# Kernel optimization log

Hardware: AMD Instinct MI355X
Metric: run time of the kernel (lower is better)

Reference implementation:

```python
import jax, jax.numpy as jnp
import numpy as np

EPS = 1e-5

def conv1d_same(x, w, b):
    # x: [B,C,T], w: [O,I,K], b: [O]
    y = jax.lax.conv_general_dilated(x, w, window_strides=(1,), padding='SAME',
                                     dimension_numbers=('NCH', 'OIH', 'NCH'))
    return y + b[None, :, None]

def bn_eval(x, gamma, beta):
    # running_mean=0, running_var=1 (fresh BatchNorm1d in eval mode)
    inv = 1.0 / jnp.sqrt(1.0 + EPS)
    return x * (gamma * inv)[None, :, None] + beta[None, :, None]

def gelu(x):
    return jax.nn.gelu(x, approximate=False)

def conv_block(x, c1w, c1b, c2w, c2b, g1, be1, g2, be2, skw=None, skb=None):
    res = x if skw is None else jnp.einsum('bct,oc->bot', x, skw[:, :, 0]) + skb[None, :, None]
    h = gelu(bn_eval(conv1d_same(x, c1w, c1b), g1, be1))
    h = bn_eval(conv1d_same(h, c2w, c2b), g2, be2)
    return gelu(h + res)

def setup_inputs() -> dict:
    key = jax.random.key(0)
    ks = jax.random.split(key, 32)
    B, C, T = 1024, 271, 281
    H, H2, E, NCLS, NSUBJ = 128, 256, 16, 1854, 4
    g = lambda i, shape, s=0.02: jax.random.normal(ks[i], shape, dtype=jnp.float32) * s
    inp = {}
    inp['X'] = jax.random.normal(ks[0], (B, C, T), dtype=jnp.float32)
    inp['subject_idxs'] = jax.random.randint(ks[1], (B,), 0, NSUBJ, dtype=jnp.int32)
    inp['attention'] = jax.random.normal(ks[2], (C, C), dtype=jnp.float32)
    inp['sa_w'] = g(3, (H, C), 0.05)
    inp['sa_b'] = jnp.zeros((H,), jnp.float32)
    inp['subj_w'] = g(4, (NSUBJ, H, H), 0.05)
    inp['subj_b'] = jnp.zeros((NSUBJ, H), jnp.float32)
    # block1: 128->128 (identity skip)
    inp['b1_c1w'] = g(5, (H, H, 3)); inp['b1_c1b'] = jnp.zeros((H,), jnp.float32)
    inp['b1_c2w'] = g(6, (H, H, 3)); inp['b1_c2b'] = jnp.zeros((H,), jnp.float32)
    inp['b1_g1'] = jnp.ones((H,), jnp.float32); inp['b1_be1'] = jnp.zeros((H,), jnp.float32)
    inp['b1_g2'] = jnp.ones((H,), jnp.float32); inp['b1_be2'] = jnp.zeros((H,), jnp.float32)
    # block2: 128->256 (1x1 conv skip)
    inp['b2_c1w'] = g(7, (H2, H, 3)); inp['b2_c1b'] = jnp.zeros((H2,), jnp.float32)
    inp['b2_c2w'] = g(8, (H2, H2, 3)); inp['b2_c2b'] = jnp.zeros((H2,), jnp.float32)
    inp['b2_g1'] = jnp.ones((H2,), jnp.float32); inp['b2_be1'] = jnp.zeros((H2,), jnp.float32)
    inp['b2_g2'] = jnp.ones((H2,), jnp.float32); inp['b2_be2'] = jnp.zeros((H2,), jnp.float32)
    inp['b2_skw'] = g(9, (H2, H, 1)); inp['b2_skb'] = jnp.zeros((H2,), jnp.float32)
    # block3: 256->256 (identity skip)
    inp['b3_c1w'] = g(10, (H2, H2, 3)); inp['b3_c1b'] = jnp.zeros((H2,), jnp.float32)
    inp['b3_c2w'] = g(11, (H2, H2, 3)); inp['b3_c2b'] = jnp.zeros((H2,), jnp.float32)
    inp['b3_g1'] = jnp.ones((H2,), jnp.float32); inp['b3_be1'] = jnp.zeros((H2,), jnp.float32)
    inp['b3_g2'] = jnp.ones((H2,), jnp.float32); inp['b3_be2'] = jnp.zeros((H2,), jnp.float32)
    # subject embedding + head
    inp['emb'] = g(12, (NSUBJ, E), 1.0)
    inp['head_w1'] = g(13, (H, H2 + E), 0.05); inp['head_b1'] = jnp.zeros((H,), jnp.float32)
    inp['head_w2'] = g(14, (NCLS, H), 0.05); inp['head_b2'] = jnp.zeros((NCLS,), jnp.float32)
    return inp

def reference(X, subject_idxs, attention, sa_w, sa_b, subj_w, subj_b,
              b1_c1w, b1_c1b, b1_c2w, b1_c2b, b1_g1, b1_be1, b1_g2, b1_be2,
              b2_c1w, b2_c1b, b2_c2w, b2_c2b, b2_g1, b2_be1, b2_g2, b2_be2, b2_skw, b2_skb,
              b3_c1w, b3_c1b, b3_c2w, b3_c2b, b3_g1, b3_be1, b3_g2, b3_be2,
              emb, head_w1, head_b1, head_w2, head_b2):
    # SpatialAttention
    attn = jax.nn.softmax(attention, axis=1)            # [C,C]
    x = jnp.einsum('bct,ic->bit', X, attn)              # [B,C,T]
    x = jnp.einsum('bit,oi->bot', x, sa_w) + sa_b[None, :, None]  # [B,H,T]
    # Per-subject 1x1 conv: batched gather of weights instead of python loop
    Ws = subj_w[subject_idxs]                           # [B,H,H]
    bs = subj_b[subject_idxs]                           # [B,H]
    x = jnp.einsum('bct,boc->bot', x, Ws) + bs[:, :, None]
    # ConvBlock stack
    x = conv_block(x, b1_c1w, b1_c1b, b1_c2w, b1_c2b, b1_g1, b1_be1, b1_g2, b1_be2)
    x = conv_block(x, b2_c1w, b2_c1b, b2_c2w, b2_c2b, b2_g1, b2_be1, b2_g2, b2_be2, b2_skw, b2_skb)
    x = conv_block(x, b3_c1w, b3_c1b, b3_c2w, b3_c2b, b3_g1, b3_be1, b3_g2, b3_be2)
    # Head: global avg pool over time, concat subject embedding, MLP
    x = jnp.mean(x, axis=2)                             # [B,2H]
    x = jnp.concatenate([x, emb[subject_idxs]], axis=1) # [B,2H+E]
    h = jax.nn.relu(x @ head_w1.T + head_b1)
    return h @ head_w2.T + head_b2                      # [B,num_classes]
```

## Files before the change

kernel.cpp:

```cpp
#include <hip/hip_runtime.h>
#include <hip/hip_bf16.h>
#include <math.h>

constexpr int Bz = 1024;
constexpr int C0 = 271;
constexpr int CP0 = 288;
constexpr int Tt = 281;
constexpr int TR = 292;
constexpr int H1 = 128;
constexpr int H2 = 256;
constexpr int NCLS = 1854;
constexpr int ED = 16;
constexpr float BN_INV = 0.9999950000374996f;

typedef __attribute__((ext_vector_type(8))) short s16x8;
typedef __attribute__((ext_vector_type(16))) float f32x16;

__device__ __forceinline__ float gelu_f(float v) {
    return 0.5f * v * (1.0f + erff(v * 0.7071067811865475f));
}
__device__ __forceinline__ float bf2f(short s) {
    return __builtin_bit_cast(float, ((unsigned int)(unsigned short)s) << 16);
}
__device__ __forceinline__ short f2bf(float f) {
    return __builtin_bit_cast(short, __float2bfloat16(f));
}

typedef unsigned int u32;
typedef const __attribute__((address_space(1))) u32 gu32;
typedef __attribute__((address_space(3))) u32 lu32;

__device__ __forceinline__ void gl16(const void* g, void* l) {
    __builtin_amdgcn_global_load_lds((gu32*)(uintptr_t)g, (lu32*)(uintptr_t)l, 16, 0, 0);
}
template<int N> __device__ __forceinline__ void waitv() {
    asm volatile("s_waitcnt vmcnt(%0)" :: "i"(N) : "memory");
}
__device__ __forceinline__ void hard_barrier() {
    __builtin_amdgcn_s_barrier();
    __builtin_amdgcn_sched_barrier(0);
}


__global__ void zrows_k(short* base, int C) {
    const int b = blockIdx.x;
    const int n = 11 * (C / 8);
    for (int i = threadIdx.x; i < n; i += 256) {
        int ri = i / (C / 8), c8 = i - ri * (C / 8);
        int row = (ri == 0) ? 0 : 281 + ri;
        *(int4*)(base + ((size_t)b * TR + row) * C + c8 * 8) = make_int4(0, 0, 0, 0);
    }
}

__global__ void softmax_rows_k(const float* __restrict__ a, float* __restrict__ o, int n) {
    __shared__ float red[256];
    const int row = blockIdx.x, tid = threadIdx.x;
    const float* r = a + (size_t)row * n;
    float m = -1e30f;
    for (int i = tid; i < n; i += 256) m = fmaxf(m, r[i]);
    red[tid] = m; __syncthreads();
    for (int s = 128; s > 0; s >>= 1) { if (tid < s) red[tid] = fmaxf(red[tid], red[tid + s]); __syncthreads(); }
    m = red[0]; __syncthreads();
    float acc = 0.f;
    for (int i = tid; i < n; i += 256) acc += expf(r[i] - m);
    red[tid] = acc; __syncthreads();
    for (int s = 128; s > 0; s >>= 1) { if (tid < s) red[tid] += red[tid + s]; __syncthreads(); }
    const float inv = 1.0f / red[0];
    for (int i = tid; i < n; i += 256) o[(size_t)row * n + i] = expf(r[i] - m) * inv;
}

__global__ void gemm_M_k(const float* __restrict__ sa_w, const float* __restrict__ attnS,
                         float* __restrict__ M) {
    int idx = blockIdx.x * 256 + threadIdx.x;
    if (idx >= H1 * C0) return;
    int o = idx / C0, c = idx - o * C0;
    float s = 0.f;
    for (int i = 0; i < C0; ++i) s = fmaf(sa_w[(size_t)o * C0 + i], attnS[(size_t)i * C0 + c], s);
    M[idx] = s;
}

__global__ void wfrag_k(const float* __restrict__ w, short* __restrict__ out,
                        int CIN, int O, int K, int NC) {
    int idx = blockIdx.x * 256 + threadIdx.x;
    int OB32 = O / 32;
    int total = NC * K * OB32 * 2 * 512;
    if (idx >= total) return;
    int j = idx & 7, lane = (idx >> 3) & 63, kk = (idx >> 9) & 1, r = idx >> 10;
    int ob = r % OB32, r2 = r / OB32;
    int k = r2 % K, cc = r2 / K;
    int o = ob * 32 + (lane & 31);
    int c = cc * 32 + kk * 16 + (lane >> 5) * 8 + j;
    float v = (c < CIN) ? w[((size_t)o * CIN + c) * K + k] : 0.f;
    out[idx] = f2bf(v);
}

__global__ void msubA_k(const float* __restrict__ subj_w, const float* __restrict__ M,
                        short* __restrict__ out) {
    int idx = blockIdx.x * 256 + threadIdx.x;
    const int per_s = 9 * 1 * 4 * 2 * 512;
    if (idx >= 4 * per_s) return;
    int s = idx / per_s, rem = idx % per_s;
    int j = rem & 7, lane = (rem >> 3) & 63, kk = (rem >> 9) & 1, r = rem >> 10;
    int ob = r % 4, cc = r / 4;
    int o = ob * 32 + (lane & 31);
    int c = cc * 32 + kk * 16 + (lane >> 5) * 8 + j;
    float a = 0.f;
    if (c < C0) {
        const float* wr = subj_w + ((size_t)s * 128 + o) * 128;
        for (int h = 0; h < 128; ++h) a = fmaf(wr[h], M[(size_t)h * C0 + c], a);
    }
    out[idx] = f2bf(a);
}

__global__ void biasS_k(const float* __restrict__ subj_w, const float* __restrict__ sa_b,
                        const float* __restrict__ subj_b, float* __restrict__ biasS) {
    int idx = blockIdx.x * 256 + threadIdx.x;
    if (idx >= 4 * H1) return;
    int s = idx >> 7, o = idx & 127;
    const float* wr = subj_w + ((size_t)s * H1 + o) * H1;
    float a = subj_b[idx];
    for (int h = 0; h < H1; ++h) a = fmaf(wr[h], sa_b[h], a);
    biasS[idx] = a;
}

__global__ void xpose_k(const float* __restrict__ X, short* __restrict__ xT) {
    __shared__ float tile[32][33];
    int b = blockIdx.z;
    int t0 = blockIdx.x * 32, c0 = blockIdx.y * 32;
    int tx = threadIdx.x, ty = threadIdx.y;
    #pragma unroll
    for (int i = 0; i < 4; ++i) {
        int c = c0 + ty + i * 8, t = t0 + tx;
        float v = 0.f;
        if (c < C0 && t < Tt) v = X[((size_t)b * C0 + c) * Tt + t];
        tile[ty + i * 8][tx] = v;
    }
    __syncthreads();
    #pragma unroll
    for (int i = 0; i < 4; ++i) {
        int t = t0 + ty + i * 8, c = c0 + tx;
        if (t < Tt) xT[((size_t)b * TR + t + 1) * CP0 + c] = f2bf(tile[tx][ty + i * 8]);
    }
}


template<int NCCp, int ROWUp, int NW, int NCH>
__device__ __forceinline__ void convFS_stage(
    const short* slabg, int XC, int cubase, char* lds, int wv, int lane)
{
    constexpr int ROWB = ROWUp * 16;
    for (int i = wv; i < NCH; i += NW) {
        int pos = i * 1024 + lane * 16;
        int rl = pos / ROWB;
        int up = (pos - rl * ROWB) >> 4;
        if (rl > 291) rl = 291;
        int ul = up ^ (rl & 7);
        int srcu = (ul < NCCp * 4) ? ul : 0;
        gl16(slabg + (size_t)rl * XC + (cubase + srcu) * 8, lds + i * 1024);
    }
}

template<int K, int NCCp, int ROWUp, int OB32>
__device__ __forceinline__ void convFS_compute(
    f32x16 (&acc)[2][3], const short* __restrict__ wb, const char* Xb,
    int ccbase, int tg, int lane, int l31, int hi, int wvo)
{
    constexpr int ROWB = ROWUp * 16;
    constexpr int ROFF = 1 - (K - 1) / 2;
    #pragma unroll
    for (int cc = 0; cc < NCCp; ++cc) {
        s16x8 a[2][K][2];
        #pragma unroll
        for (int os = 0; os < 2; ++os)
            #pragma unroll
            for (int k = 0; k < K; ++k)
                #pragma unroll
                for (int kk = 0; kk < 2; ++kk) {
                    int ci = (((ccbase + cc) * K + k) * OB32 + wvo * 2 + os) * 2 + kk;
                    a[os][k][kk] = *(const s16x8*)(wb + (size_t)ci * 512 + lane * 8);
                }
        #pragma unroll
        for (int k = 0; k < K; ++k)
            #pragma unroll
            for (int kk = 0; kk < 2; ++kk)
                #pragma unroll
                for (int ts = 0; ts < 3; ++ts) {
                    int rl = tg + ts * 32 + l31 + k + ROFF;
                    s16x8 bv = *(const s16x8*)(Xb + (size_t)rl * ROWB +
                        (((cc * 4 + (kk << 1) + hi) ^ (rl & 7)) << 4));
                    acc[0][ts] = __builtin_amdgcn_mfma_f32_32x32x16_bf16(a[0][k][kk], bv, acc[0][ts], 0, 0, 0);
                    acc[1][ts] = __builtin_amdgcn_mfma_f32_32x32x16_bf16(a[1][k][kk], bv, acc[1][ts], 0, 0, 0);
                }
    }
}

template<int K, int NCC_A, int ROWU_A, int NCC_B, int ROWU_B,
         int O_BLK, int NOW, int NB, bool GELU, bool HASRES>
__global__ __launch_bounds__(NOW * NB * 192)
void convFS(const short* __restrict__ xin, int XC,
            const short* __restrict__ wfrag,
            const float* __restrict__ bias,
            const float* __restrict__ gamma, const float* __restrict__ beta,
            const short* __restrict__ res, short* __restrict__ out,
            const int* __restrict__ sidx, int wsub, int bsub)
{
    constexpr int NW    = NOW * NB * 3;
    constexpr int NT    = NW * 64;
    constexpr int OB32  = O_BLK / 32;
    constexpr int SLABB = ((292 * ROWU_A * 16) + 1023) & ~1023;
    constexpr int NCH_A = SLABB / 1024;
    constexpr int NCH_B = (292 * ROWU_B * 16 + 1023) / 1024;
    constexpr int O2    = O_BLK * 2;

    __shared__ __align__(16) char smem[NB * SLABB];

    const int b0   = blockIdx.x * NB;
    const int tid  = threadIdx.x;
    const int lane = tid & 63, wv = tid >> 6;
    const int l31  = lane & 31, hi = lane >> 5;
    const int bqw  = wv / (NOW * 3);
    const int w2   = wv % (NOW * 3);
    const int wvt  = w2 / NOW;
    const int wvo  = w2 % NOW;
    const int tg   = wvt * 96;

    int subj = sidx ? sidx[b0] : 0;
    const short* wb = wfrag + (size_t)subj * wsub;
    const float* bb = bias + (size_t)subj * bsub;

    f32x16 acc[2][3];
    #pragma unroll
    for (int i = 0; i < 2; ++i)
        #pragma unroll
        for (int j = 0; j < 3; ++j)
            #pragma unroll
            for (int e = 0; e < 16; ++e) acc[i][j][e] = 0.f;

    #pragma unroll
    for (int b = 0; b < NB; ++b)
        convFS_stage<NCC_A, ROWU_A, NW, NCH_A>(
            xin + (size_t)(b0 + b) * TR * XC, XC, 0, smem + b * SLABB, wv, lane);
    waitv<0>();
    hard_barrier();

    const char* Xb = smem + bqw * SLABB;
    convFS_compute<K, NCC_A, ROWU_A, OB32>(acc, wb, Xb, 0, tg, lane, l31, hi, wvo);

    if constexpr (NCC_B > 0) {
        hard_barrier();
        #pragma unroll
        for (int b = 0; b < NB; ++b)
            convFS_stage<NCC_B, ROWU_B, NW, NCH_B>(
                xin + (size_t)(b0 + b) * TR * XC, XC, NCC_A * 4, smem + b * SLABB, wv, lane);
        waitv<0>();
        hard_barrier();
        convFS_compute<K, NCC_B, ROWU_B, OB32>(acc, wb, Xb, NCC_A, tg, lane, l31, hi, wvo);
    }

    constexpr int RCH = O_BLK / 8;
    for (int g = 0; g < 3; ++g) {
        __syncthreads();
        if (wvt == g) {
            #pragma unroll
            for (int os = 0; os < 2; ++os) {
                #pragma unroll
                for (int rq = 0; rq < 4; ++rq) {
                    #pragma unroll
                    for (int rp = 0; rp < 2; ++rp) {
                        const int oc = wvo * 64 + os * 32 + 8 * rq + rp * 2 + 4 * hi;
                        const float bv0 = bb[oc], bv1 = bb[oc + 1];
                        const float g0 = gamma ? gamma[oc] * BN_INV : 1.f;
                        const float g1 = gamma ? gamma[oc + 1] * BN_INV : 1.f;
                        const float e0 = beta ? beta[oc] : 0.f;
                        const float e1 = beta ? beta[oc + 1] : 0.f;
                        const int r0 = rq * 4 + rp * 2;
                        #pragma unroll
                        for (int ts = 0; ts < 3; ++ts) {
                            float v0 = (acc[os][ts][r0] + bv0) * g0 + e0;
                            float v1 = (acc[os][ts][r0 + 1] + bv1) * g1 + e1;
                            int tl = ts * 32 + l31;
                            int byte = (bqw * 96 + tl) * O2 + ((oc * 2) ^ ((tl & 15) << 4));
                            __hip_bfloat162 pk;
                            pk.x = __float2bfloat16(v0);
                            pk.y = __float2bfloat16(v1);
                            *(__hip_bfloat162*)(smem + byte) = pk;
                        }
                    }
                }
            }
        }
        __syncthreads();
        for (int qq = tid; qq < NB * 96 * RCH; qq += NT) {
            int bql = qq / (96 * RCH), rem = qq - bql * (96 * RCH);
            int r = rem / RCH, cp = rem - r * RCH;
            int t = g * 96 + r;
            if (t >= Tt) continue;
            s16x8 hv = *(const s16x8*)(smem + (bql * 96 + r) * O2 + ((cp * 16) ^ ((r & 15) << 4)));
            size_t orow = ((size_t)(b0 + bql) * TR + t + 1) * O_BLK + cp * 8;
            s16x8 rv;
            if (HASRES) rv = *(const s16x8*)(res + orow);
            s16x8 ov;
            #pragma unroll
            for (int j = 0; j < 8; ++j) {
                float v = bf2f(hv[j]);
                if (HASRES) v += bf2f(rv[j]);
                if (GELU) v = gelu_f(v);
                ov[j] = f2bf(v);
            }
            *(s16x8*)(out + orow) = ov;
        }
    }
}


__global__ void poolCL_k(const short* __restrict__ x, float* __restrict__ pooled) {
    const int b = blockIdx.x;
    const int o = threadIdx.x;
    const short* p = x + ((size_t)b * TR + 1) * H2 + o;
    float s = 0.f;
    for (int t = 0; t < Tt; ++t) s += bf2f(p[(size_t)t * H2]);
    pooled[(size_t)b * H2 + o] = s * (1.0f / Tt);
}

__global__ void head1_k(const float* __restrict__ pooled, const float* __restrict__ emb,
                        const int* __restrict__ sidx, const float* __restrict__ w1,
                        const float* __restrict__ b1, float* __restrict__ hout) {
    int idx = blockIdx.x * 256 + threadIdx.x;
    if (idx >= Bz * H1) return;
    int b = idx >> 7, j = idx & 127;
    const float* wr = w1 + (size_t)j * (H2 + ED);
    const float* pr = pooled + (size_t)b * H2;
    float a = b1[j];
    for (int i = 0; i < H2; ++i) a = fmaf(pr[i], wr[i], a);
    const float* er = emb + (size_t)sidx[b] * ED;
    #pragma unroll
    for (int e = 0; e < ED; ++e) a = fmaf(er[e], wr[H2 + e], a);
    hout[idx] = fmaxf(a, 0.f);
}

__global__ __launch_bounds__(256)
void head2_k(const float* __restrict__ h, const float* __restrict__ w2,
             const float* __restrict__ b2, float* __restrict__ out) {
    const int n0 = blockIdx.x * 64;
    const int b0 = blockIdx.y * 16;
    __shared__ float hs[16][128];
    __shared__ float w2s[64][129];
    const int tid = threadIdx.x;
    for (int idx = tid; idx < 16 * 128; idx += 256) {
        int bl = idx >> 7, j = idx & 127;
        hs[bl][j] = h[(size_t)(b0 + bl) * H1 + j];
    }
    for (int idx = tid; idx < 64 * 128; idx += 256) {
        int nl = idx >> 7, j = idx & 127;
        int n = n0 + nl;
        w2s[nl][j] = (n < NCLS) ? w2[(size_t)n * H1 + j] : 0.f;
    }
    __syncthreads();
    const int nl = tid & 63, bg = tid >> 6;
    float acc[4] = {0.f, 0.f, 0.f, 0.f};
    for (int j = 0; j < 128; ++j) {
        const float wv = w2s[nl][j];
        #pragma unroll
        for (int bb = 0; bb < 4; ++bb) acc[bb] = fmaf(wv, hs[bg * 4 + bb][j], acc[bb]);
    }
    const int n = n0 + nl;
    if (n < NCLS) {
        const float bv = b2[n];
        #pragma unroll
        for (int bb = 0; bb < 4; ++bb)
            out[(size_t)(b0 + bg * 4 + bb) * NCLS + n] = acc[bb] + bv;
    }
}


extern "C" void kernel_launch(void* const* d_in, const int* in_sizes, int n_in,
                              void* d_out, int out_size, void* d_ws, size_t ws_size,
                              hipStream_t stream) {
    const float* X      = (const float*)d_in[0];
    const int*   sidx   = (const int*)  d_in[1];
    const float* attn   = (const float*)d_in[2];
    const float* sa_w   = (const float*)d_in[3];
    const float* sa_b   = (const float*)d_in[4];
    const float* subj_w = (const float*)d_in[5];
    const float* subj_b = (const float*)d_in[6];
    const float* b1c1w = (const float*)d_in[7];  const float* b1c1b = (const float*)d_in[8];
    const float* b1c2w = (const float*)d_in[9];  const float* b1c2b = (const float*)d_in[10];
    const float* b1g1  = (const float*)d_in[11]; const float* b1be1 = (const float*)d_in[12];
    const float* b1g2  = (const float*)d_in[13]; const float* b1be2 = (const float*)d_in[14];
    const float* b2c1w = (const float*)d_in[15]; const float* b2c1b = (const float*)d_in[16];
    const float* b2c2w = (const float*)d_in[17]; const float* b2c2b = (const float*)d_in[18];
    const float* b2g1  = (const float*)d_in[19]; const float* b2be1 = (const float*)d_in[20];
    const float* b2g2  = (const float*)d_in[21]; const float* b2be2 = (const float*)d_in[22];
    const float* b2skw = (const float*)d_in[23]; const float* b2skb = (const float*)d_in[24];
    const float* b3c1w = (const float*)d_in[25]; const float* b3c1b = (const float*)d_in[26];
    const float* b3c2w = (const float*)d_in[27]; const float* b3c2b = (const float*)d_in[28];
    const float* b3g1  = (const float*)d_in[29]; const float* b3be1 = (const float*)d_in[30];
    const float* b3g2  = (const float*)d_in[31]; const float* b3be2 = (const float*)d_in[32];
    const float* emb   = (const float*)d_in[33];
    const float* hw1   = (const float*)d_in[34]; const float* hb1 = (const float*)d_in[35];
    const float* hw2   = (const float*)d_in[36]; const float* hb2 = (const float*)d_in[37];
    float* out = (float*)d_out;
    (void)in_sizes; (void)n_in; (void)out_size; (void)ws_size;

    char* wsp = (char*)d_ws;
    size_t off = 0;
    auto allocF = [&](size_t n) {
        float* p = (float*)(wsp + off);
        off += ((n * sizeof(float)) + 255) & ~(size_t)255;
        return p;
    };
    auto allocS = [&](size_t n) {
        short* p = (short*)(wsp + off);
        off += ((n * sizeof(short)) + 255) & ~(size_t)255;
        return p;
    };
    float* attnS   = allocF((size_t)C0 * C0);
    float* Mmat    = allocF((size_t)H1 * C0);
    float* biasS   = allocF((size_t)4 * H1);
    float* pooled  = allocF((size_t)Bz * H2);
    float* hbuf    = allocF((size_t)Bz * H1);
    short* wStageA = allocS((size_t)4 * 9 * 4 * 2 * 512);
    short* wp_b1c1 = allocS((size_t)4 * 3 * 4 * 2 * 512);
    short* wp_b1c2 = allocS((size_t)4 * 3 * 4 * 2 * 512);
    short* wp_skip = allocS((size_t)4 * 1 * 8 * 2 * 512);
    short* wp_b2c1 = allocS((size_t)4 * 3 * 8 * 2 * 512);
    short* wp_b2c2 = allocS((size_t)8 * 3 * 8 * 2 * 512);
    short* wp_b3c1 = allocS((size_t)8 * 3 * 8 * 2 * 512);
    short* wp_b3c2 = allocS((size_t)8 * 3 * 8 * 2 * 512);
    short* xT   = allocS((size_t)Bz * TR * CP0);
    short* bufP = allocS((size_t)Bz * TR * H1);
    short* bufQ = allocS((size_t)Bz * TR * H1);
    short* bufR = allocS((size_t)Bz * TR * H2);
    short* bufS = allocS((size_t)Bz * TR * H2);

    zrows_k<<<Bz, 256, 0, stream>>>(xT, CP0);
    zrows_k<<<Bz, 256, 0, stream>>>(bufP, H1);
    zrows_k<<<Bz, 256, 0, stream>>>(bufQ, H1);
    zrows_k<<<Bz, 256, 0, stream>>>(bufR, H2);
    zrows_k<<<Bz, 256, 0, stream>>>(bufS, H2);

    softmax_rows_k<<<C0, 256, 0, stream>>>(attn, attnS, C0);
    gemm_M_k<<<(H1 * C0 + 255) / 256, 256, 0, stream>>>(sa_w, attnS, Mmat);
    msubA_k<<<(4 * 36864 + 255) / 256, 256, 0, stream>>>(subj_w, Mmat, wStageA);
    biasS_k<<<2, 256, 0, stream>>>(subj_w, sa_b, subj_b, biasS);
    wfrag_k<<<(4*3*4*2*512 + 255) / 256, 256, 0, stream>>>(b1c1w, wp_b1c1, 128, 128, 3, 4);
    wfrag_k<<<(4*3*4*2*512 + 255) / 256, 256, 0, stream>>>(b1c2w, wp_b1c2, 128, 128, 3, 4);
    wfrag_k<<<(4*1*8*2*512 + 255) / 256, 256, 0, stream>>>(b2skw, wp_skip, 128, 256, 1, 4);
    wfrag_k<<<(4*3*8*2*512 + 255) / 256, 256, 0, stream>>>(b2c1w, wp_b2c1, 128, 256, 3, 4);
    wfrag_k<<<(8*3*8*2*512 + 255) / 256, 256, 0, stream>>>(b2c2w, wp_b2c2, 256, 256, 3, 8);
    wfrag_k<<<(8*3*8*2*512 + 255) / 256, 256, 0, stream>>>(b3c1w, wp_b3c1, 256, 256, 3, 8);
    wfrag_k<<<(8*3*8*2*512 + 255) / 256, 256, 0, stream>>>(b3c2w, wp_b3c2, 256, 256, 3, 8);
    xpose_k<<<dim3(9, 9, Bz), dim3(32, 8), 0, stream>>>(X, xT);

    convFS<1, 5, 24, 4, 16, 128, 2, 1, false, false><<<Bz, 384, 0, stream>>>(
        xT, CP0, wStageA, biasS, nullptr, nullptr, nullptr, bufP, sidx, 36864, 128);
    convFS<3, 4, 16, 0, 0, 128, 2, 2, true, false><<<Bz / 2, 768, 0, stream>>>(
        bufP, H1, wp_b1c1, b1c1b, b1g1, b1be1, nullptr, bufQ, nullptr, 0, 0);
    convFS<3, 4, 16, 0, 0, 128, 2, 2, true, true><<<Bz / 2, 768, 0, stream>>>(
        bufQ, H1, wp_b1c2, b1c2b, b1g2, b1be2, bufP, bufP, nullptr, 0, 0);
    convFS<1, 4, 16, 0, 0, 256, 4, 1, false, false><<<Bz, 768, 0, stream>>>(
        bufP, H1, wp_skip, b2skb, nullptr, nullptr, nullptr, bufS, nullptr, 0, 0);
    convFS<3, 4, 16, 0, 0, 256, 4, 1, true, false><<<Bz, 768, 0, stream>>>(
        bufP, H1, wp_b2c1, b2c1b, b2g1, b2be1, nullptr, bufR, nullptr, 0, 0);
    convFS<3, 8, 32, 0, 0, 256, 4, 1, true, true><<<Bz, 768, 0, stream>>>(
        bufR, H2, wp_b2c2, b2c2b, b2g2, b2be2, bufS, bufS, nullptr, 0, 0);
    convFS<3, 8, 32, 0, 0, 256, 4, 1, true, false><<<Bz, 768, 0, stream>>>(
        bufS, H2, wp_b3c1, b3c1b, b3g1, b3be1, nullptr, bufR, nullptr, 0, 0);
    convFS<3, 8, 32, 0, 0, 256, 4, 1, true, true><<<Bz, 768, 0, stream>>>(
        bufR, H2, wp_b3c2, b3c2b, b3g2, b3be2, bufS, bufS, nullptr, 0, 0);

    poolCL_k<<<Bz, 256, 0, stream>>>(bufS, pooled);
    head1_k<<<(Bz * H1 + 255) / 256, 256, 0, stream>>>(pooled, emb, sidx, hw1, hb1, hbuf);
    head2_k<<<dim3((NCLS + 63) / 64, Bz / 16), 256, 0, stream>>>(hbuf, hw2, hb2, out);
}
```

Baseline: 1.370 ms.

## Tile conv kernels over time chunks and fuse final conv with average pooling

Replaces the whole-sequence conv kernel with a kernel that splits each sample's time axis into three 96-step tiles on a second grid dimension, so each block stages only a 104-row halo slab in LDS. This uses smaller blocks with a launch bound of two per CU to raise occupancy, and issues the MFMA sequences under raised wave priority. The first stage now covers all input channels in a single pass, with weights padded to 10 chunks. The last conv folds global average pooling into its epilogue through shuffle reductions and atomicAdd into a zeroed buffer, removing the separate pool kernel and the final activation write. The cost is reloading overlapping halo rows across tiles and float atomics that make the pooled sum order nondeterministic.

```diff
diff --git a/kernel.cpp b/kernel.cpp
--- a/kernel.cpp
+++ b/kernel.cpp
@@ -50,6 +50,11 @@
         int row = (ri == 0) ? 0 : 281 + ri;
         *(int4*)(base + ((size_t)b * TR + row) * C + c8 * 8) = make_int4(0, 0, 0, 0);
     }
+}
+
+__global__ void zerof_k(float* p, int n) {
+    int i = blockIdx.x * 256 + threadIdx.x;
+    if (i < n) p[i] = 0.f;
 }
 
 __global__ void softmax_rows_k(const float* __restrict__ a, float* __restrict__ o, int n) {
@@ -97,7 +102,7 @@
 __global__ void msubA_k(const float* __restrict__ subj_w, const float* __restrict__ M,
                         short* __restrict__ out) {
     int idx = blockIdx.x * 256 + threadIdx.x;
-    const int per_s = 9 * 1 * 4 * 2 * 512;
+    const int per_s = 10 * 1 * 4 * 2 * 512;
     if (idx >= 4 * per_s) return;
     int s = idx / per_s, rem = idx % per_s;
     int j = rem & 7, lane = (rem >> 3) & 63, kk = (rem >> 9) & 1, r = rem >> 10;
@@ -144,183 +149,184 @@
 }
 
 
-template<int NCCp, int ROWUp, int NW, int NCH>
-__device__ __forceinline__ void convFS_stage(
-    const short* slabg, int XC, int cubase, char* lds, int wv, int lane)
-{
-    constexpr int ROWB = ROWUp * 16;
-    for (int i = wv; i < NCH; i += NW) {
-        int pos = i * 1024 + lane * 16;
-        int rl = pos / ROWB;
-        int up = (pos - rl * ROWB) >> 4;
-        if (rl > 291) rl = 291;
-        int ul = up ^ (rl & 7);
-        int srcu = (ul < NCCp * 4) ? ul : 0;
-        gl16(slabg + (size_t)rl * XC + (cubase + srcu) * 8, lds + i * 1024);
-    }
-}
-
-template<int K, int NCCp, int ROWUp, int OB32>
-__device__ __forceinline__ void convFS_compute(
-    f32x16 (&acc)[2][3], const short* __restrict__ wb, const char* Xb,
-    int ccbase, int tg, int lane, int l31, int hi, int wvo)
-{
-    constexpr int ROWB = ROWUp * 16;
-    constexpr int ROFF = 1 - (K - 1) / 2;
-    #pragma unroll
-    for (int cc = 0; cc < NCCp; ++cc) {
-        s16x8 a[2][K][2];
-        #pragma unroll
-        for (int os = 0; os < 2; ++os)
-            #pragma unroll
-            for (int k = 0; k < K; ++k)
-                #pragma unroll
-                for (int kk = 0; kk < 2; ++kk) {
-                    int ci = (((ccbase + cc) * K + k) * OB32 + wvo * 2 + os) * 2 + kk;
-                    a[os][k][kk] = *(const s16x8*)(wb + (size_t)ci * 512 + lane * 8);
-                }
-        #pragma unroll
-        for (int k = 0; k < K; ++k)
-            #pragma unroll
-            for (int kk = 0; kk < 2; ++kk)
-                #pragma unroll
-                for (int ts = 0; ts < 3; ++ts) {
-                    int rl = tg + ts * 32 + l31 + k + ROFF;
-                    s16x8 bv = *(const s16x8*)(Xb + (size_t)rl * ROWB +
-                        (((cc * 4 + (kk << 1) + hi) ^ (rl & 7)) << 4));
-                    acc[0][ts] = __builtin_amdgcn_mfma_f32_32x32x16_bf16(a[0][k][kk], bv, acc[0][ts], 0, 0, 0);
-                    acc[1][ts] = __builtin_amdgcn_mfma_f32_32x32x16_bf16(a[1][k][kk], bv, acc[1][ts], 0, 0, 0);
-                }
-    }
-}
-
-template<int K, int NCC_A, int ROWU_A, int NCC_B, int ROWU_B,
-         int O_BLK, int NOW, int NB, bool GELU, bool HASRES>
-__global__ __launch_bounds__(NOW * NB * 192)
-void convFS(const short* __restrict__ xin, int XC,
-            const short* __restrict__ wfrag,
+template<int K, int NCC, int O_BLK, int NB, bool GELU, bool HASRES, bool POOL>
+__global__ __launch_bounds__(NB * (O_BLK / 64) * 64, 2)
+void convPL(const short* __restrict__ xin, int XC,
+            const short* __restrict__ wfragp,
             const float* __restrict__ bias,
             const float* __restrict__ gamma, const float* __restrict__ beta,
-            const short* __restrict__ res, short* __restrict__ out,
+            const short* __restrict__ res, short* __restrict__ outp,
+            float* __restrict__ pooled,
             const int* __restrict__ sidx, int wsub, int bsub)
 {
-    constexpr int NW    = NOW * NB * 3;
-    constexpr int NT    = NW * 64;
-    constexpr int OB32  = O_BLK / 32;
-    constexpr int SLABB = ((292 * ROWU_A * 16) + 1023) & ~1023;
-    constexpr int NCH_A = SLABB / 1024;
-    constexpr int NCH_B = (292 * ROWU_B * 16 + 1023) / 1024;
-    constexpr int O2    = O_BLK * 2;
-
-    __shared__ __align__(16) char smem[NB * SLABB];
-
-    const int b0   = blockIdx.x * NB;
+    constexpr int OW   = O_BLK / 64;
+    constexpr int NW   = NB * OW;
+    constexpr int NT   = NW * 64;
+    constexpr int OB32 = O_BLK / 32;
+    constexpr int ROWB = NCC * 64;
+    constexpr int CH   = 104 * ROWB / 1024;
+    constexpr int OUTB = 96 * O_BLK * 2;
+    constexpr int SLAB = CH * 1024;
+    constexpr int REG  = SLAB > OUTB ? SLAB : OUTB;
+    constexpr int O2   = O_BLK * 2;
+
+    __shared__ __align__(16) char smem[NB * REG];
+
+    const int t0   = blockIdx.x * 96;
+    const int b0   = blockIdx.y * NB;
     const int tid  = threadIdx.x;
     const int lane = tid & 63, wv = tid >> 6;
     const int l31  = lane & 31, hi = lane >> 5;
-    const int bqw  = wv / (NOW * 3);
-    const int w2   = wv % (NOW * 3);
-    const int wvt  = w2 / NOW;
-    const int wvo  = w2 % NOW;
-    const int tg   = wvt * 96;
+    const int bq   = wv / OW;
+    const int wvo  = wv % OW;
 
     int subj = sidx ? sidx[b0] : 0;
-    const short* wb = wfrag + (size_t)subj * wsub;
+    const short* wb = wfragp + (size_t)subj * wsub;
     const float* bb = bias + (size_t)subj * bsub;
 
-    f32x16 acc[2][3];
-    #pragma unroll
-    for (int i = 0; i < 2; ++i)
-        #pragma unroll
-        for (int j = 0; j < 3; ++j)
-            #pragma unroll
-            for (int e = 0; e < 16; ++e) acc[i][j][e] = 0.f;
-
-    #pragma unroll
-    for (int b = 0; b < NB; ++b)
-        convFS_stage<NCC_A, ROWU_A, NW, NCH_A>(
-            xin + (size_t)(b0 + b) * TR * XC, XC, 0, smem + b * SLABB, wv, lane);
+    for (int i = wv; i < NB * CH; i += NW) {
+        int bql = i / CH, ic = i - bql * CH;
+        int pos = ic * 1024 + lane * 16;
+        int rl  = pos / ROWB;
+        int u   = (pos - rl * ROWB) >> 4;
+        int usrc = u ^ (rl & 7);
+        int br  = t0 + rl;
+        if (br > 291) br = 291;
+        gl16(xin + ((size_t)(b0 + bql) * TR + br) * XC + usrc * 8,
+             smem + bql * REG + ic * 1024);
+    }
     waitv<0>();
     hard_barrier();
 
-    const char* Xb = smem + bqw * SLABB;
-    convFS_compute<K, NCC_A, ROWU_A, OB32>(acc, wb, Xb, 0, tg, lane, l31, hi, wvo);
-
-    if constexpr (NCC_B > 0) {
-        hard_barrier();
-        #pragma unroll
-        for (int b = 0; b < NB; ++b)
-            convFS_stage<NCC_B, ROWU_B, NW, NCH_B>(
-                xin + (size_t)(b0 + b) * TR * XC, XC, NCC_A * 4, smem + b * SLABB, wv, lane);
-        waitv<0>();
-        hard_barrier();
-        convFS_compute<K, NCC_B, ROWU_B, OB32>(acc, wb, Xb, NCC_A, tg, lane, l31, hi, wvo);
-    }
-
-    constexpr int RCH = O_BLK / 8;
-    for (int g = 0; g < 3; ++g) {
-        __syncthreads();
-        if (wvt == g) {
-            #pragma unroll
-            for (int os = 0; os < 2; ++os) {
+    f32x16 acc[2][3];
+    #pragma unroll
+    for (int i = 0; i < 2; ++i)
+        #pragma unroll
+        for (int j = 0; j < 3; ++j)
+            #pragma unroll
+            for (int e = 0; e < 16; ++e) acc[i][j][e] = 0.f;
+
+    const char* Xb = smem + bq * REG;
+
+    #pragma unroll
+    for (int cc = 0; cc < NCC; ++cc) {
+        #pragma unroll
+        for (int k = 0; k < K; ++k) {
+            #pragma unroll
+            for (int kk = 0; kk < 2; ++kk) {
+                const short* ap = wb + ((size_t)((((cc * K + k) * OB32 + wvo * 2) * 2) + kk)) * 512;
+                s16x8 a0 = *(const s16x8*)(ap + lane * 8);
+                s16x8 a1 = *(const s16x8*)(ap + 1024 + lane * 8);
+                __builtin_amdgcn_s_setprio(1);
                 #pragma unroll
-                for (int rq = 0; rq < 4; ++rq) {
-                    #pragma unroll
-                    for (int rp = 0; rp < 2; ++rp) {
-                        const int oc = wvo * 64 + os * 32 + 8 * rq + rp * 2 + 4 * hi;
-                        const float bv0 = bb[oc], bv1 = bb[oc + 1];
-                        const float g0 = gamma ? gamma[oc] * BN_INV : 1.f;
-                        const float g1 = gamma ? gamma[oc + 1] * BN_INV : 1.f;
-                        const float e0 = beta ? beta[oc] : 0.f;
-                        const float e1 = beta ? beta[oc + 1] : 0.f;
-                        const int r0 = rq * 4 + rp * 2;
-                        #pragma unroll
-                        for (int ts = 0; ts < 3; ++ts) {
-                            float v0 = (acc[os][ts][r0] + bv0) * g0 + e0;
-                            float v1 = (acc[os][ts][r0 + 1] + bv1) * g1 + e1;
-                            int tl = ts * 32 + l31;
-                            int byte = (bqw * 96 + tl) * O2 + ((oc * 2) ^ ((tl & 15) << 4));
-                            __hip_bfloat162 pk;
-                            pk.x = __float2bfloat16(v0);
-                            pk.y = __float2bfloat16(v1);
-                            *(__hip_bfloat162*)(smem + byte) = pk;
-                        }
-                    }
+                for (int ts = 0; ts < 3; ++ts) {
+                    int rl = ts * 32 + l31 + k;
+                    s16x8 bv = *(const s16x8*)(Xb + rl * ROWB +
+                                (((cc * 4 + kk * 2 + hi) ^ (rl & 7)) << 4));
+                    acc[0][ts] = __builtin_amdgcn_mfma_f32_32x32x16_bf16(a0, bv, acc[0][ts], 0, 0, 0);
+                    acc[1][ts] = __builtin_amdgcn_mfma_f32_32x32x16_bf16(a1, bv, acc[1][ts], 0, 0, 0);
+                }
+                __builtin_amdgcn_s_setprio(0);
+            }
+        }
+    }
+
+    const int b = b0 + bq;
+
+    if constexpr (POOL) {
+        float ps[2][16];
+        #pragma unroll
+        for (int os = 0; os < 2; ++os)
+            #pragma unroll
+            for (int rg = 0; rg < 16; ++rg) ps[os][rg] = 0.f;
+        #pragma unroll
+        for (int os = 0; os < 2; ++os) {
+            #pragma unroll
+            for (int rg = 0; rg < 16; ++rg) {
+                const int oc = wvo * 64 + os * 32 + (rg & 3) + 8 * (rg >> 2) + 4 * hi;
+                const float bv = bb[oc];
+                const float g0 = gamma ? gamma[oc] * BN_INV : 1.f;
+                const float e0 = beta ? beta[oc] : 0.f;
+                #pragma unroll
+                for (int ts = 0; ts < 3; ++ts) {
+                    int t = t0 + ts * 32 + l31;
+                    float v = (acc[os][ts][rg] + bv) * g0 + e0;
+                    if (HASRES) v += bf2f(res[((size_t)b * TR + t + 1) * O_BLK + oc]);
+                    if (GELU) v = gelu_f(v);
+                    if (t < Tt) ps[os][rg] += v;
                 }
             }
         }
-        __syncthreads();
-        for (int qq = tid; qq < NB * 96 * RCH; qq += NT) {
-            int bql = qq / (96 * RCH), rem = qq - bql * (96 * RCH);
-            int r = rem / RCH, cp = rem - r * RCH;
-            int t = g * 96 + r;
-            if (t >= Tt) continue;
-            s16x8 hv = *(const s16x8*)(smem + (bql * 96 + r) * O2 + ((cp * 16) ^ ((r & 15) << 4)));
-            size_t orow = ((size_t)(b0 + bql) * TR + t + 1) * O_BLK + cp * 8;
-            s16x8 rv;
-            if (HASRES) rv = *(const s16x8*)(res + orow);
-            s16x8 ov;
-            #pragma unroll
-            for (int j = 0; j < 8; ++j) {
-                float v = bf2f(hv[j]);
-                if (HASRES) v += bf2f(rv[j]);
-                if (GELU) v = gelu_f(v);
-                ov[j] = f2bf(v);
+        #pragma unroll
+        for (int os = 0; os < 2; ++os) {
+            #pragma unroll
+            for (int rg = 0; rg < 16; ++rg) {
+                float s = ps[os][rg];
+                s += __shfl_xor(s, 1);
+                s += __shfl_xor(s, 2);
+                s += __shfl_xor(s, 4);
+                s += __shfl_xor(s, 8);
+                s += __shfl_xor(s, 16);
+                if (l31 == 0) {
+                    const int oc = wvo * 64 + os * 32 + (rg & 3) + 8 * (rg >> 2) + 4 * hi;
+                    atomicAdd(pooled + (size_t)b * H2 + oc, s * (1.0f / 281.0f));
+                }
             }
-            *(s16x8*)(out + orow) = ov;
         }
-    }
-}
-
-
-__global__ void poolCL_k(const short* __restrict__ x, float* __restrict__ pooled) {
-    const int b = blockIdx.x;
-    const int o = threadIdx.x;
-    const short* p = x + ((size_t)b * TR + 1) * H2 + o;
-    float s = 0.f;
-    for (int t = 0; t < Tt; ++t) s += bf2f(p[(size_t)t * H2]);
-    pooled[(size_t)b * H2 + o] = s * (1.0f / Tt);
-}
+        return;
+    }
+
+    __syncthreads();
+    #pragma unroll
+    for (int os = 0; os < 2; ++os) {
+        #pragma unroll
+        for (int rq = 0; rq < 4; ++rq) {
+            #pragma unroll
+            for (int rp = 0; rp < 2; ++rp) {
+                const int oc = wvo * 64 + os * 32 + 8 * rq + rp * 2 + 4 * hi;
+                const float bv0 = bb[oc], bv1 = bb[oc + 1];
+                const float g0 = gamma ? gamma[oc] * BN_INV : 1.f;
+                const float g1 = gamma ? gamma[oc + 1] * BN_INV : 1.f;
+                const float e0 = beta ? beta[oc] : 0.f;
+                const float e1 = beta ? beta[oc + 1] : 0.f;
+                const int r0 = rq * 4 + rp * 2;
+                #pragma unroll
+                for (int ts = 0; ts < 3; ++ts) {
+                    float v0 = (acc[os][ts][r0] + bv0) * g0 + e0;
+                    float v1 = (acc[os][ts][r0 + 1] + bv1) * g1 + e1;
+                    int tl = ts * 32 + l31;
+                    int byte = (bq * 96 + tl) * O2 + ((oc * 2) ^ ((tl & 15) << 4));
+                    __hip_bfloat162 pk;
+                    pk.x = __float2bfloat16(v0);
+                    pk.y = __float2bfloat16(v1);
+                    *(__hip_bfloat162*)(smem + byte) = pk;
+                }
+            }
+        }
+    }
+    __syncthreads();
+    constexpr int RCH = O_BLK / 8;
+    for (int qq = tid; qq < NB * 96 * RCH; qq += NT) {
+        int bql = qq / (96 * RCH), rem = qq - bql * (96 * RCH);
+        int r = rem / RCH, cp = rem - r * RCH;
+        int t = t0 + r;
+        if (t >= Tt) continue;
+        s16x8 hv = *(const s16x8*)(smem + (bql * 96 + r) * O2 + ((cp * 16) ^ ((r & 15) << 4)));
+        size_t orow = ((size_t)(b0 + bql) * TR + t + 1) * O_BLK + cp * 8;
+        s16x8 rv;
+        if (HASRES) rv = *(const s16x8*)(res + orow);
+        s16x8 ov;
+        #pragma unroll
+        for (int j = 0; j < 8; ++j) {
+            float v = bf2f(hv[j]);
+            if (HASRES) v += bf2f(rv[j]);
+            if (GELU) v = gelu_f(v);
+            ov[j] = f2bf(v);
+        }
+        *(s16x8*)(outp + orow) = ov;
+    }
+}
+
 
 __global__ void head1_k(const float* __restrict__ pooled, const float* __restrict__ emb,
                         const int* __restrict__ sidx, const float* __restrict__ w1,
@@ -419,7 +425,7 @@
     float* biasS   = allocF((size_t)4 * H1);
     float* pooled  = allocF((size_t)Bz * H2);
     float* hbuf    = allocF((size_t)Bz * H1);
-    short* wStageA = allocS((size_t)4 * 9 * 4 * 2 * 512);
+    short* wStageA = allocS((size_t)4 * 10 * 4 * 2 * 512);
     short* wp_b1c1 = allocS((size_t)4 * 3 * 4 * 2 * 512);
     short* wp_b1c2 = allocS((size_t)4 * 3 * 4 * 2 * 512);
     short* wp_skip = allocS((size_t)4 * 1 * 8 * 2 * 512);
@@ -427,7 +433,7 @@
     short* wp_b2c2 = allocS((size_t)8 * 3 * 8 * 2 * 512);
     short* wp_b3c1 = allocS((size_t)8 * 3 * 8 * 2 * 512);
     short* wp_b3c2 = allocS((size_t)8 * 3 * 8 * 2 * 512);
-    short* xT   = allocS((size_t)Bz * TR * CP0);
+    short* xT   = allocS((size_t)Bz * TR * CP0 + 64);
     short* bufP = allocS((size_t)Bz * TR * H1);
     short* bufQ = allocS((size_t)Bz * TR * H1);
     short* bufR = allocS((size_t)Bz * TR * H2);
@@ -438,10 +444,11 @@
     zrows_k<<<Bz, 256, 0, stream>>>(bufQ, H1);
     zrows_k<<<Bz, 256, 0, stream>>>(bufR, H2);
     zrows_k<<<Bz, 256, 0, stream>>>(bufS, H2);
+    zerof_k<<<(Bz * H2 + 255) / 256, 256, 0, stream>>>(pooled, Bz * H2);
 
     softmax_rows_k<<<C0, 256, 0, stream>>>(attn, attnS, C0);
     gemm_M_k<<<(H1 * C0 + 255) / 256, 256, 0, stream>>>(sa_w, attnS, Mmat);
-    msubA_k<<<(4 * 36864 + 255) / 256, 256, 0, stream>>>(subj_w, Mmat, wStageA);
+    msubA_k<<<(4 * 40960 + 255) / 256, 256, 0, stream>>>(subj_w, Mmat, wStageA);
     biasS_k<<<2, 256, 0, stream>>>(subj_w, sa_b, subj_b, biasS);
     wfrag_k<<<(4*3*4*2*512 + 255) / 256, 256, 0, stream>>>(b1c1w, wp_b1c1, 128, 128, 3, 4);
     wfrag_k<<<(4*3*4*2*512 + 255) / 256, 256, 0, stream>>>(b1c2w, wp_b1c2, 128, 128, 3, 4);
@@ -452,24 +459,23 @@
     wfrag_k<<<(8*3*8*2*512 + 255) / 256, 256, 0, stream>>>(b3c2w, wp_b3c2, 256, 256, 3, 8);
     xpose_k<<<dim3(9, 9, Bz), dim3(32, 8), 0, stream>>>(X, xT);
 
-    convFS<1, 5, 24, 4, 16, 128, 2, 1, false, false><<<Bz, 384, 0, stream>>>(
-        xT, CP0, wStageA, biasS, nullptr, nullptr, nullptr, bufP, sidx, 36864, 128);
-    convFS<3, 4, 16, 0, 0, 128, 2, 2, true, false><<<Bz / 2, 768, 0, stream>>>(
-        bufP, H1, wp_b1c1, b1c1b, b1g1, b1be1, nullptr, bufQ, nullptr, 0, 0);
-    convFS<3, 4, 16, 0, 0, 128, 2, 2, true, true><<<Bz / 2, 768, 0, stream>>>(
-        bufQ, H1, wp_b1c2, b1c2b, b1g2, b1be2, bufP, bufP, nullptr, 0, 0);
-    convFS<1, 4, 16, 0, 0, 256, 4, 1, false, false><<<Bz, 768, 0, stream>>>(
-        bufP, H1, wp_skip, b2skb, nullptr, nullptr, nullptr, bufS, nullptr, 0, 0);
-    convFS<3, 4, 16, 0, 0, 256, 4, 1, true, false><<<Bz, 768, 0, stream>>>(
-        bufP, H1, wp_b2c1, b2c1b, b2g1, b2be1, nullptr, bufR, nullptr, 0, 0);
-    convFS<3, 8, 32, 0, 0, 256, 4, 1, true, true><<<Bz, 768, 0, stream>>>(
-        bufR, H2, wp_b2c2, b2c2b, b2g2, b2be2, bufS, bufS, nullptr, 0, 0);
-    convFS<3, 8, 32, 0, 0, 256, 4, 1, true, false><<<Bz, 768, 0, stream>>>(
-        bufS, H2, wp_b3c1, b3c1b, b3g1, b3be1, nullptr, bufR, nullptr, 0, 0);
-    convFS<3, 8, 32, 0, 0, 256, 4, 1, true, true><<<Bz, 768, 0, stream>>>(
-        bufR, H2, wp_b3c2, b3c2b, b3g2, b3be2, bufS, bufS, nullptr, 0, 0);
-
-    poolCL_k<<<Bz, 256, 0, stream>>>(bufS, pooled);
+    convPL<1, 10, 128, 1, false, false, false><<<dim3(3, Bz), 128, 0, stream>>>(
+        xT, CP0, wStageA, biasS, nullptr, nullptr, nullptr, bufP, nullptr, sidx, 40960, 128);
+    convPL<3, 4, 128, 2, true, false, false><<<dim3(3, Bz / 2), 256, 0, stream>>>(
+        bufP, H1, wp_b1c1, b1c1b, b1g1, b1be1, nullptr, bufQ, nullptr, nullptr, 0, 0);
+    convPL<3, 4, 128, 2, true, true, false><<<dim3(3, Bz / 2), 256, 0, stream>>>(
+        bufQ, H1, wp_b1c2, b1c2b, b1g2, b1be2, bufP, bufP, nullptr, nullptr, 0, 0);
+    convPL<1, 4, 256, 1, false, false, false><<<dim3(3, Bz), 256, 0, stream>>>(
+        bufP, H1, wp_skip, b2skb, nullptr, nullptr, nullptr, bufS, nullptr, nullptr, 0, 0);
+    convPL<3, 4, 256, 1, true, false, false><<<dim3(3, Bz), 256, 0, stream>>>(
+        bufP, H1, wp_b2c1, b2c1b, b2g1, b2be1, nullptr, bufR, nullptr, nullptr, 0, 0);
+    convPL<3, 8, 256, 1, true, true, false><<<dim3(3, Bz), 256, 0, stream>>>(
+        bufR, H2, wp_b2c2, b2c2b, b2g2, b2be2, bufS, bufS, nullptr, nullptr, 0, 0);
+    convPL<3, 8, 256, 1, true, false, false><<<dim3(3, Bz), 256, 0, stream>>>(
+        bufS, H2, wp_b3c1, b3c1b, b3g1, b3be1, nullptr, bufR, nullptr, nullptr, 0, 0);
+    convPL<3, 8, 256, 1, true, true, true><<<dim3(3, Bz), 256, 0, stream>>>(
+        bufR, H2, wp_b3c2, b3c2b, b3g2, b3be2, bufS, nullptr, pooled, nullptr, 0, 0);
+
     head1_k<<<(Bz * H1 + 255) / 256, 256, 0, stream>>>(pooled, emb, sidx, hw1, hb1, hbuf);
     head2_k<<<dim3((NCLS + 63) / 64, Bz / 16), 256, 0, stream>>>(hbuf, hw2, hb2, out);
 }
```

Result: slower. 1.499 ms (+9.4%).

## Phase-pipeline conv MFMA loop with weight prefetch and fuse final pooling

Applied to the files above, without the earlier changes.

Restructures the conv compute loop into per-(channel-chunk, tap) phases. Each phase double-buffers the weight fragments for the next phase, loads the LDS operands, then issues MFMAs between barriers with raised wave priority. This is meant to hide weight-load latency and interleave waves better. Separately, the last conv's epilogue now accumulates the time-mean directly into pooled instead of writing bufS, which drops the poolCL kernel and a full activation write and read. The extra per-phase barriers add sync cost, and the pooled reduction assumes NB=1 and reuses shared memory.

```diff
diff --git a/kernel.cpp b/kernel.cpp
--- a/kernel.cpp
+++ b/kernel.cpp
@@ -37,6 +37,7 @@
     asm volatile("s_waitcnt vmcnt(%0)" :: "i"(N) : "memory");
 }
 __device__ __forceinline__ void hard_barrier() {
+    __builtin_amdgcn_sched_barrier(0);
     __builtin_amdgcn_s_barrier();
     __builtin_amdgcn_sched_barrier(0);
 }
@@ -145,7 +146,7 @@
 
 
 template<int NCCp, int ROWUp, int NW, int NCH>
-__device__ __forceinline__ void convFS_stage(
+__device__ __forceinline__ void conv_stage(
     const short* slabg, int XC, int cubase, char* lds, int wv, int lane)
 {
     constexpr int ROWB = ROWUp * 16;
@@ -160,48 +161,63 @@
     }
 }
 
-template<int K, int NCCp, int ROWUp, int OB32>
-__device__ __forceinline__ void convFS_compute(
+template<int K, int CCB, int NPH, int ROWU, int OB32>
+__device__ __forceinline__ void conv_phases(
     f32x16 (&acc)[2][3], const short* __restrict__ wb, const char* Xb,
-    int ccbase, int tg, int lane, int l31, int hi, int wvo)
+    int tg, int lane, int l31, int hi, int wvo)
 {
-    constexpr int ROWB = ROWUp * 16;
+    constexpr int ROWB = ROWU * 16;
     constexpr int ROFF = 1 - (K - 1) / 2;
-    #pragma unroll
-    for (int cc = 0; cc < NCCp; ++cc) {
-        s16x8 a[2][K][2];
-        #pragma unroll
-        for (int os = 0; os < 2; ++os)
+    s16x8 ab[2][4];
+    #pragma unroll
+    for (int i = 0; i < 4; ++i) {
+        int ci = ((CCB * K + 0) * OB32 + wvo * 2 + (i >> 1)) * 2 + (i & 1);
+        ab[0][i] = *(const s16x8*)(wb + (size_t)ci * 512 + lane * 8);
+    }
+    #pragma unroll
+    for (int p = 0; p < NPH; ++p) {
+        const int k  = p % K;
+        const int cl = p / K;
+        if (p + 1 < NPH) {
+            const int cn = CCB + (p + 1) / K, kn = (p + 1) % K;
             #pragma unroll
-            for (int k = 0; k < K; ++k)
-                #pragma unroll
-                for (int kk = 0; kk < 2; ++kk) {
-                    int ci = (((ccbase + cc) * K + k) * OB32 + wvo * 2 + os) * 2 + kk;
-                    a[os][k][kk] = *(const s16x8*)(wb + (size_t)ci * 512 + lane * 8);
-                }
-        #pragma unroll
-        for (int k = 0; k < K; ++k)
+            for (int i = 0; i < 4; ++i) {
+                int ci = ((cn * K + kn) * OB32 + wvo * 2 + (i >> 1)) * 2 + (i & 1);
+                ab[(p + 1) & 1][i] = *(const s16x8*)(wb + (size_t)ci * 512 + lane * 8);
+            }
+        }
+        s16x8 bf[2][3];
+        #pragma unroll
+        for (int kk = 0; kk < 2; ++kk)
             #pragma unroll
-            for (int kk = 0; kk < 2; ++kk)
-                #pragma unroll
-                for (int ts = 0; ts < 3; ++ts) {
-                    int rl = tg + ts * 32 + l31 + k + ROFF;
-                    s16x8 bv = *(const s16x8*)(Xb + (size_t)rl * ROWB +
-                        (((cc * 4 + (kk << 1) + hi) ^ (rl & 7)) << 4));
-                    acc[0][ts] = __builtin_amdgcn_mfma_f32_32x32x16_bf16(a[0][k][kk], bv, acc[0][ts], 0, 0, 0);
-                    acc[1][ts] = __builtin_amdgcn_mfma_f32_32x32x16_bf16(a[1][k][kk], bv, acc[1][ts], 0, 0, 0);
-                }
+            for (int ts = 0; ts < 3; ++ts) {
+                int rl = tg + ts * 32 + l31 + k + ROFF;
+                bf[kk][ts] = *(const s16x8*)(Xb + (size_t)rl * ROWB +
+                               (((cl * 4 + kk * 2 + hi) ^ (rl & 7)) << 4));
+            }
+        hard_barrier();
+        __builtin_amdgcn_s_setprio(1);
+        #pragma unroll
+        for (int ts = 0; ts < 3; ++ts)
+            #pragma unroll
+            for (int kk = 0; kk < 2; ++kk) {
+                acc[0][ts] = __builtin_amdgcn_mfma_f32_32x32x16_bf16(ab[p & 1][kk],     bf[kk][ts], acc[0][ts], 0, 0, 0);
+                acc[1][ts] = __builtin_amdgcn_mfma_f32_32x32x16_bf16(ab[p & 1][2 + kk], bf[kk][ts], acc[1][ts], 0, 0, 0);
+            }
+        __builtin_amdgcn_s_setprio(0);
+        hard_barrier();
     }
 }
 
 template<int K, int NCC_A, int ROWU_A, int NCC_B, int ROWU_B,
-         int O_BLK, int NOW, int NB, bool GELU, bool HASRES>
+         int O_BLK, int NOW, int NB, bool GELU, bool HASRES, bool POOL>
 __global__ __launch_bounds__(NOW * NB * 192)
-void convFS(const short* __restrict__ xin, int XC,
+void convPH(const short* __restrict__ xin, int XC,
             const short* __restrict__ wfrag,
             const float* __restrict__ bias,
             const float* __restrict__ gamma, const float* __restrict__ beta,
-            const short* __restrict__ res, short* __restrict__ out,
+            const short* __restrict__ res, short* __restrict__ outp,
+            float* __restrict__ pooled,
             const int* __restrict__ sidx, int wsub, int bsub)
 {
     constexpr int NW    = NOW * NB * 3;
@@ -238,26 +254,30 @@
 
     #pragma unroll
     for (int b = 0; b < NB; ++b)
-        convFS_stage<NCC_A, ROWU_A, NW, NCH_A>(
+        conv_stage<NCC_A, ROWU_A, NW, NCH_A>(
             xin + (size_t)(b0 + b) * TR * XC, XC, 0, smem + b * SLABB, wv, lane);
     waitv<0>();
     hard_barrier();
 
     const char* Xb = smem + bqw * SLABB;
-    convFS_compute<K, NCC_A, ROWU_A, OB32>(acc, wb, Xb, 0, tg, lane, l31, hi, wvo);
+    conv_phases<K, 0, NCC_A * K, ROWU_A, OB32>(acc, wb, Xb, tg, lane, l31, hi, wvo);
 
     if constexpr (NCC_B > 0) {
-        hard_barrier();
         #pragma unroll
         for (int b = 0; b < NB; ++b)
-            convFS_stage<NCC_B, ROWU_B, NW, NCH_B>(
+            conv_stage<NCC_B, ROWU_B, NW, NCH_B>(
                 xin + (size_t)(b0 + b) * TR * XC, XC, NCC_A * 4, smem + b * SLABB, wv, lane);
         waitv<0>();
         hard_barrier();
-        convFS_compute<K, NCC_B, ROWU_B, OB32>(acc, wb, Xb, NCC_A, tg, lane, l31, hi, wvo);
+        conv_phases<K, NCC_A, NCC_B * K, ROWU_B, OB32>(acc, wb, Xb, tg, lane, l31, hi, wvo);
     }
 
     constexpr int RCH = O_BLK / 8;
+    float ps[8];
+    if constexpr (POOL) {
+        #pragma unroll
+        for (int j = 0; j < 8; ++j) ps[j] = 0.f;
+    }
     for (int g = 0; g < 3; ++g) {
         __syncthreads();
         if (wvt == g) {
@@ -299,28 +319,44 @@
             size_t orow = ((size_t)(b0 + bql) * TR + t + 1) * O_BLK + cp * 8;
             s16x8 rv;
             if (HASRES) rv = *(const s16x8*)(res + orow);
-            s16x8 ov;
-            #pragma unroll
-            for (int j = 0; j < 8; ++j) {
-                float v = bf2f(hv[j]);
-                if (HASRES) v += bf2f(rv[j]);
-                if (GELU) v = gelu_f(v);
-                ov[j] = f2bf(v);
+            if constexpr (POOL) {
+                #pragma unroll
+                for (int j = 0; j < 8; ++j) {
+                    float v = bf2f(hv[j]);
+                    if (HASRES) v += bf2f(rv[j]);
+                    if (GELU) v = gelu_f(v);
+                    ps[j] += v;
+                }
+            } else {
+                s16x8 ov;
+                #pragma unroll
+                for (int j = 0; j < 8; ++j) {
+                    float v = bf2f(hv[j]);
+                    if (HASRES) v += bf2f(rv[j]);
+                    if (GELU) v = gelu_f(v);
+                    ov[j] = f2bf(v);
+                }
+                *(s16x8*)(outp + orow) = ov;
             }
-            *(s16x8*)(out + orow) = ov;
         }
     }
-}
-
-
-__global__ void poolCL_k(const short* __restrict__ x, float* __restrict__ pooled) {
-    const int b = blockIdx.x;
-    const int o = threadIdx.x;
-    const short* p = x + ((size_t)b * TR + 1) * H2 + o;
-    float s = 0.f;
-    for (int t = 0; t < Tt; ++t) s += bf2f(p[(size_t)t * H2]);
-    pooled[(size_t)b * H2 + o] = s * (1.0f / Tt);
-}
+
+    if constexpr (POOL) {
+        constexpr int NRED = NT / RCH;
+        float* part = (float*)(smem + 96 * (size_t)O2);
+        __syncthreads();
+        #pragma unroll
+        for (int j = 0; j < 8; ++j) part[tid * 8 + j] = ps[j];
+        __syncthreads();
+        if (tid < O_BLK) {
+            int cp = tid >> 3, j = tid & 7;
+            float s = 0.f;
+            for (int r = 0; r < NRED; ++r) s += part[(cp + RCH * r) * 8 + j];
+            pooled[(size_t)b0 * H2 + tid] = s * (1.0f / 281.0f);
+        }
+    }
+}
+
 
 __global__ void head1_k(const float* __restrict__ pooled, const float* __restrict__ emb,
                         const int* __restrict__ sidx, const float* __restrict__ w1,
@@ -427,7 +463,7 @@
     short* wp_b2c2 = allocS((size_t)8 * 3 * 8 * 2 * 512);
     short* wp_b3c1 = allocS((size_t)8 * 3 * 8 * 2 * 512);
     short* wp_b3c2 = allocS((size_t)8 * 3 * 8 * 2 * 512);
-    short* xT   = allocS((size_t)Bz * TR * CP0);
+    short* xT   = allocS((size_t)Bz * TR * CP0 + 64);
     short* bufP = allocS((size_t)Bz * TR * H1);
     short* bufQ = allocS((size_t)Bz * TR * H1);
     short* bufR = allocS((size_t)Bz * TR * H2);
@@ -452,24 +488,23 @@
     wfrag_k<<<(8*3*8*2*512 + 255) / 256, 256, 0, stream>>>(b3c2w, wp_b3c2, 256, 256, 3, 8);
     xpose_k<<<dim3(9, 9, Bz), dim3(32, 8), 0, stream>>>(X, xT);
 
-    convFS<1, 5, 24, 4, 16, 128, 2, 1, false, false><<<Bz, 384, 0, stream>>>(
-        xT, CP0, wStageA, biasS, nullptr, nullptr, nullptr, bufP, sidx, 36864, 128);
-    convFS<3, 4, 16, 0, 0, 128, 2, 2, true, false><<<Bz / 2, 768, 0, stream>>>(
-        bufP, H1, wp_b1c1, b1c1b, b1g1, b1be1, nullptr, bufQ, nullptr, 0, 0);
-    convFS<3, 4, 16, 0, 0, 128, 2, 2, true, true><<<Bz / 2, 768, 0, stream>>>(
-        bufQ, H1, wp_b1c2, b1c2b, b1g2, b1be2, bufP, bufP, nullptr, 0, 0);
-    convFS<1, 4, 16, 0, 0, 256, 4, 1, false, false><<<Bz, 768, 0, stream>>>(
-        bufP, H1, wp_skip, b2skb, nullptr, nullptr, nullptr, bufS, nullptr, 0, 0);
-    convFS<3, 4, 16, 0, 0, 256, 4, 1, true, false><<<Bz, 768, 0, stream>>>(
-        bufP, H1, wp_b2c1, b2c1b, b2g1, b2be1, nullptr, bufR, nullptr, 0, 0);
-    convFS<3, 8, 32, 0, 0, 256, 4, 1, true, true><<<Bz, 768, 0, stream>>>(
-        bufR, H2, wp_b2c2, b2c2b, b2g2, b2be2, bufS, bufS, nullptr, 0, 0);
-    convFS<3, 8, 32, 0, 0, 256, 4, 1, true, false><<<Bz, 768, 0, stream>>>(
-        bufS, H2, wp_b3c1, b3c1b, b3g1, b3be1, nullptr, bufR, nullptr, 0, 0);
-    convFS<3, 8, 32, 0, 0, 256, 4, 1, true, true><<<Bz, 768, 0, stream>>>(
-        bufR, H2, wp_b3c2, b3c2b, b3g2, b3be2, bufS, bufS, nullptr, 0, 0);
-
-    poolCL_k<<<Bz, 256, 0, stream>>>(bufS, pooled);
+    convPH<1, 5, 24, 4, 16, 128, 2, 1, false, false, false><<<Bz, 384, 0, stream>>>(
+        xT, CP0, wStageA, biasS, nullptr, nullptr, nullptr, bufP, nullptr, sidx, 36864, 128);
+    convPH<3, 4, 16, 0, 0, 128, 2, 2, true, false, false><<<Bz / 2, 768, 0, stream>>>(
+        bufP, H1, wp_b1c1, b1c1b, b1g1, b1be1, nullptr, bufQ, nullptr, nullptr, 0, 0);
+    convPH<3, 4, 16, 0, 0, 128, 2, 2, true, true, false><<<Bz / 2, 768, 0, stream>>>(
+        bufQ, H1, wp_b1c2, b1c2b, b1g2, b1be2, bufP, bufP, nullptr, nullptr, 0, 0);
+    convPH<1, 4, 16, 0, 0, 256, 4, 1, false, false, false><<<Bz, 768, 0, stream>>>(
+        bufP, H1, wp_skip, b2skb, nullptr, nullptr, nullptr, bufS, nullptr, nullptr, 0, 0);
+    convPH<3, 4, 16, 0, 0, 256, 4, 1, true, false, false><<<Bz, 768, 0, stream>>>(
+        bufP, H1, wp_b2c1, b2c1b, b2g1, b2be1, nullptr, bufR, nullptr, nullptr, 0, 0);
+    convPH<3, 8, 32, 0, 0, 256, 4, 1, true, true, false><<<Bz, 768, 0, stream>>>(
+        bufR, H2, wp_b2c2, b2c2b, b2g2, b2be2, bufS, bufS, nullptr, nullptr, 0, 0);
+    convPH<3, 8, 32, 0, 0, 256, 4, 1, true, false, false><<<Bz, 768, 0, stream>>>(
+        bufS, H2, wp_b3c1, b3c1b, b3g1, b3be1, nullptr, bufR, nullptr, nullptr, 0, 0);
+    convPH<3, 8, 32, 0, 0, 256, 4, 1, true, true, true><<<Bz, 768, 0, stream>>>(
+        bufR, H2, wp_b3c2, b3c2b, b3g2, b3be2, bufS, nullptr, pooled, nullptr, 0, 0);
+
     head1_k<<<(Bz * H1 + 255) / 256, 256, 0, stream>>>(pooled, emb, sidx, hw1, hb1, hbuf);
     head2_k<<<dim3((NCLS + 63) / 64, Bz / 16), 256, 0, stream>>>(hbuf, hw2, hb2, out);
 }
```

Measured after the change: 1.367 ms. About the same (-0.2%).
